# Kernel optimization log

Measured on AMD Instinct MI355X. Metric: run time of the kernel, lower is better.

## Reference

```python
import jax, jax.numpy as jnp
import numpy as np

B, L, IN, HID, D3 = 32, 8192, 512, 512, 128

def setup_inputs() -> dict:
    key = jax.random.key(0)
    ks = jax.random.split(key, 7)
    s_in = 1.0 / np.sqrt(IN)
    s_h = 1.0 / np.sqrt(HID)
    return {
        'inputs': jax.random.normal(ks[0], (B, IN), jnp.float32),
        'context': jax.random.normal(ks[1], (B, L, HID), jnp.float32),
        'Wi': jax.random.uniform(ks[2], (D3, IN), jnp.float32, -s_in, s_in),
        'bi': jax.random.uniform(ks[3], (D3,), jnp.float32, -s_in, s_in),
        'Wh': jax.random.uniform(ks[4], (D3, HID), jnp.float32, -s_h, s_h),
        'bh': jax.random.uniform(ks[5], (D3,), jnp.float32, -s_h, s_h),
        'V': jax.random.uniform(ks[6], (D3,), jnp.float32, -1.0, 1.0),
    }

def reference(inputs, context, Wi, bi, Wh, bh, V):
    # inputs: (B, IN) -> (B, 1, D3); context: (B, L, HID) -> (B, L, D3)
    q = (inputs @ Wi.T + bi)[:, None, :]
    k = jnp.einsum('blh,dh->bld', context, Wh) + bh
    a = jnp.tanh(q + k)                              # (B, L, D3)
    att_row = jnp.einsum('bld,d->bl', a, V)[:, None, :]  # (B, 1, L)
    # NOTE: original applies softmax over dim=1 (the singleton dim) -> all ones.
    att = jax.nn.softmax(att_row, axis=1).squeeze(1)     # (B, L), faithful quirk
    return (att_row, att)
```

## Files before the change

### kernel.cpp

```cpp
#include <hip/hip_runtime.h>

typedef __attribute__((ext_vector_type(8))) short short8;
typedef __attribute__((ext_vector_type(8))) unsigned short ushort8;
typedef __attribute__((ext_vector_type(4))) float f32x4;

#define B_   32
#define L_   8192
#define IN_  512
#define HID_ 512
#define D3_  128

static __device__ __forceinline__ short f2bf(float f) {
    return __builtin_bit_cast(short, (__bf16)f);
}
static __device__ __forceinline__ unsigned short f2bfu(float f) {
    return __builtin_bit_cast(unsigned short, (__bf16)f);
}

static __device__ __forceinline__ void gload_lds16(const void* g, void* l) {
    __builtin_amdgcn_global_load_lds(
        (const __attribute__((address_space(1))) unsigned int*)g,
        (__attribute__((address_space(3))) unsigned int*)l, 16, 0, 0);
}

__global__ void prep_whb2(const float* __restrict__ wh, unsigned short* __restrict__ whb2) {
    int u = blockIdx.x * 256 + threadIdx.x;
    int lane = u & 63;
    int nt   = (u >> 6) & 7;
    int ks   = u >> 9;
    int col  = nt * 16 + (lane & 15);
    int k0   = ks * 32 + (lane >> 4) * 8;
    const float* src = wh + col * HID_ + k0;
    float4 a = *(const float4*)(src);
    float4 b = *(const float4*)(src + 4);
    unsigned short* d = whb2 + (size_t)u * 8;
    d[0] = f2bfu(a.x); d[1] = f2bfu(a.y); d[2] = f2bfu(a.z); d[3] = f2bfu(a.w);
    d[4] = f2bfu(b.x); d[5] = f2bfu(b.y); d[6] = f2bfu(b.z); d[7] = f2bfu(b.w);
}

__global__ void prep_qpb(const float* __restrict__ inputs, const float* __restrict__ Wi,
                         const float* __restrict__ bi, const float* __restrict__ bh,
                         float* __restrict__ qpb) {
    int b = blockIdx.x;
    int d = threadIdx.x;
    float acc = bi[d] + bh[d];
    const float* xr = inputs + b * IN_;
    const float* wr = Wi + d * IN_;
    #pragma unroll 4
    for (int i = 0; i < IN_; i += 4) {
        float4 x = *(const float4*)(xr + i);
        float4 w = *(const float4*)(wr + i);
        acc += x.x * w.x + x.y * w.y + x.z * w.z + x.w * w.w;
    }
    qpb[b * D3_ + d] = acc;
}

__global__ __launch_bounds__(512) void attn_main(
    const float* __restrict__ ctx, const unsigned short* __restrict__ whb2,
    const float* __restrict__ qpb, const float* __restrict__ V,
    float* __restrict__ out)
{
    __shared__ unsigned short whs[D3_ * HID_];
    __shared__ float cbuf[2][4096];

    const int tid = threadIdx.x;

    #pragma unroll
    for (int p = 0; p < 16; ++p) {
        int m = p * 512 + tid;
        *(ushort8*)((char*)whs + (size_t)m * 16) = *(const ushort8*)(whb2 + (size_t)m * 8);
    }
    __syncthreads();

    const int lane = tid & 63;
    const int w    = tid >> 6;
    const int cb   = lane & 15;
    const int g    = lane >> 4;

    const char* bptr = (const char*)whs + lane * 16;

    const int srow = lane >> 3;
    const int spce = (lane & 7) ^ srow;
    const float* gsrcA = ctx
        + ((size_t)blockIdx.x * 1024 + w * 16 + srow) * (size_t)HID_ + spce * 4;
    const float* gsrcB = gsrcA + 8 * HID_;
    char* ldst = (char*)cbuf + w * 2048 + lane * 16;

    const char* abase = (const char*)cbuf + w * 2048 + (cb >> 3) * 1024 + (cb & 7) * 128;
    const int aoff0 = (((2 * g)     ^ (cb & 7)) << 4);
    const int aoff1 = (((2 * g + 1) ^ (cb & 7)) << 4);

    const int b = blockIdx.x >> 3;

    float vv[8], qv[8];
    #pragma unroll
    for (int nt = 0; nt < 8; ++nt) {
        vv[nt] = V[nt * 16 + cb];
        qv[nt] = qpb[b * D3_ + nt * 16 + cb];
    }

#define STAGE(CC) { \
    const size_t go_ = (size_t)((CC) >> 4) * (128 * HID_) + ((CC) & 15) * 32; \
    char* l0_ = ldst + (((CC) & 1) ? 16384 : 0); \
    gload_lds16(gsrcA + go_, l0_); \
    gload_lds16(gsrcB + go_, l0_ + 1024); }

    STAGE(0)
    STAGE(1)

    #pragma unroll 1
    for (int t = 0; t < 8; ++t) {
        f32x4 acc[8];
        #pragma unroll
        for (int nt = 0; nt < 8; ++nt) acc[nt] = (f32x4){0.f, 0.f, 0.f, 0.f};

        #pragma unroll
        for (int kk = 0; kk < 16; ++kk) {
            const int c = t * 16 + kk;
            if (c < 127) asm volatile("s_waitcnt vmcnt(2)" ::: "memory");
            else         asm volatile("s_waitcnt vmcnt(0)" ::: "memory");

            const char* ap = abase + ((c & 1) ? 16384 : 0);
            const f32x4 a0 = *(const f32x4*)(ap + aoff0);
            const f32x4 a1 = *(const f32x4*)(ap + aoff1);
            asm volatile("s_waitcnt lgkmcnt(0)" ::: "memory");
            __builtin_amdgcn_sched_barrier(0);
            if (c + 2 < 128) STAGE(c + 2)
            __builtin_amdgcn_sched_barrier(0);

            short8 aA;
            aA[0] = f2bf(a0[0]); aA[1] = f2bf(a0[1]); aA[2] = f2bf(a0[2]); aA[3] = f2bf(a0[3]);
            aA[4] = f2bf(a1[0]); aA[5] = f2bf(a1[1]); aA[6] = f2bf(a1[2]); aA[7] = f2bf(a1[3]);

            const char* bp = bptr + kk * 8192;
            #pragma unroll
            for (int nt = 0; nt < 8; ++nt) {
                const short8 bb = *(const short8*)(bp + nt * 1024);
                acc[nt] = __builtin_amdgcn_mfma_f32_16x16x32_bf16(aA, bb, acc[nt], 0, 0, 0);
            }

            if (kk == 15) {
                float s0 = 0.f, s1 = 0.f, s2 = 0.f, s3 = 0.f;
                #pragma unroll
                for (int nt = 0; nt < 8; ++nt) {
                    const float q = qv[nt], vn = vv[nt];
                    s0 += (1.f - 2.f / (__expf(2.f * (acc[nt][0] + q)) + 1.f)) * vn;
                    s1 += (1.f - 2.f / (__expf(2.f * (acc[nt][1] + q)) + 1.f)) * vn;
                    s2 += (1.f - 2.f / (__expf(2.f * (acc[nt][2] + q)) + 1.f)) * vn;
                    s3 += (1.f - 2.f / (__expf(2.f * (acc[nt][3] + q)) + 1.f)) * vn;
                }
                #pragma unroll
                for (int m = 1; m < 16; m <<= 1) {
                    s0 += __shfl_xor(s0, m, 64);
                    s1 += __shfl_xor(s1, m, 64);
                    s2 += __shfl_xor(s2, m, 64);
                    s3 += __shfl_xor(s3, m, 64);
                }
                if (cb == 0) {
                    const size_t row0 = (size_t)blockIdx.x * 1024 + (size_t)t * 128 + w * 16;
                    const size_t off_ = row0 + (size_t)g * 4;
                    *(float4*)(out + off_) = make_float4(s0, s1, s2, s3);
                    *(float4*)(out + (size_t)B_ * L_ + off_) = make_float4(1.f, 1.f, 1.f, 1.f);
                }
            }
        }
    }
#undef STAGE
}

extern "C" void kernel_launch(void* const* d_in, const int* in_sizes, int n_in,
                              void* d_out, int out_size, void* d_ws, size_t ws_size,
                              hipStream_t stream) {
    const float* inputs  = (const float*)d_in[0];
    const float* context = (const float*)d_in[1];
    const float* Wi      = (const float*)d_in[2];
    const float* bi      = (const float*)d_in[3];
    const float* Wh      = (const float*)d_in[4];
    const float* bh      = (const float*)d_in[5];
    const float* V       = (const float*)d_in[6];
    float* out = (float*)d_out;

    unsigned short* whb2 = (unsigned short*)d_ws;
    float* qpb = (float*)((char*)d_ws + (size_t)D3_ * HID_ * 2);

    prep_whb2<<<32, 256, 0, stream>>>(Wh, whb2);
    prep_qpb<<<B_, D3_, 0, stream>>>(inputs, Wi, bi, bh, qpb);
    attn_main<<<256, 512, 0, stream>>>(context, whb2, qpb, V, out);
}
```

Before: 124.6 us.

## Stream Wh weight windows through double-buffered LDS instead of preloading whole matrix

```diff
diff --git a/kernel.cpp b/kernel.cpp
--- a/kernel.cpp
+++ b/kernel.cpp
@@ -60,35 +60,29 @@
     const float* __restrict__ qpb, const float* __restrict__ V,
     float* __restrict__ out)
 {
-    __shared__ unsigned short whs[D3_ * HID_];
-    __shared__ float cbuf[2][4096];
-
-    const int tid = threadIdx.x;
-
-    #pragma unroll
-    for (int p = 0; p < 16; ++p) {
-        int m = p * 512 + tid;
-        *(ushort8*)((char*)whs + (size_t)m * 16) = *(const ushort8*)(whb2 + (size_t)m * 8);
-    }
-    __syncthreads();
-
+    __shared__ unsigned short bwin[2][16384];
+    __shared__ float cbuf[16384];
+
+    const int tid  = threadIdx.x;
     const int lane = tid & 63;
     const int w    = tid >> 6;
     const int cb   = lane & 15;
     const int g    = lane >> 4;
-
-    const char* bptr = (const char*)whs + lane * 16;
 
     const int srow = lane >> 3;
     const int spce = (lane & 7) ^ srow;
     const float* gsrcA = ctx
         + ((size_t)blockIdx.x * 1024 + w * 16 + srow) * (size_t)HID_ + spce * 4;
     const float* gsrcB = gsrcA + 8 * HID_;
-    char* ldst = (char*)cbuf + w * 2048 + lane * 16;
-
-    const char* abase = (const char*)cbuf + w * 2048 + (cb >> 3) * 1024 + (cb & 7) * 128;
+    char* ldstA = (char*)cbuf + w * 8192 + lane * 16;
+
+    const char* abase = (const char*)cbuf + w * 8192 + (cb >> 3) * 1024 + (cb & 7) * 128;
     const int aoff0 = (((2 * g)     ^ (cb & 7)) << 4);
     const int aoff1 = (((2 * g + 1) ^ (cb & 7)) << 4);
+
+    const char* bssrc = (const char*)whb2 + w * 1024 + lane * 16;
+    char* bsdst = (char*)bwin + w * 1024 + lane * 16;
+    const char* bread = (const char*)bwin + lane * 16;
 
     const int b = blockIdx.x >> 3;
 
@@ -99,73 +93,97 @@
         qv[nt] = qpb[b * D3_ + nt * 16 + cb];
     }
 
-#define STAGE(CC) { \
-    const size_t go_ = (size_t)((CC) >> 4) * (128 * HID_) + ((CC) & 15) * 32; \
-    char* l0_ = ldst + (((CC) & 1) ? 16384 : 0); \
+#define STAGE_A(CC) { \
+    const int cc_ = (CC) & 127; \
+    const size_t go_ = (size_t)(cc_ >> 4) * (128 * HID_) + (cc_ & 15) * 32; \
+    char* l0_ = ldstA + ((CC) & 3) * 2048; \
     gload_lds16(gsrcA + go_, l0_); \
     gload_lds16(gsrcB + go_, l0_ + 1024); }
 
-    STAGE(0)
-    STAGE(1)
+#define STAGE_B(WN) { \
+    const int kw_ = ((WN) & 3) * 4; \
+    char* d_ = bsdst + ((WN) & 1) * 32768; \
+    gload_lds16(bssrc + (size_t)(kw_ + 0) * 8192, d_); \
+    gload_lds16(bssrc + (size_t)(kw_ + 1) * 8192, d_ + 8192); \
+    gload_lds16(bssrc + (size_t)(kw_ + 2) * 8192, d_ + 16384); \
+    gload_lds16(bssrc + (size_t)(kw_ + 3) * 8192, d_ + 24576); }
+
+    STAGE_A(0) STAGE_A(1) STAGE_A(2) STAGE_A(3)
+    STAGE_B(0)
+    asm volatile("s_waitcnt vmcnt(8)" ::: "memory");
+    __builtin_amdgcn_s_barrier();
+
+    f32x4 acc[8];
 
     #pragma unroll 1
-    for (int t = 0; t < 8; ++t) {
-        f32x4 acc[8];
+    for (int W = 0; W < 32; ++W) {
+        if ((W & 3) == 0) {
+            #pragma unroll
+            for (int nt = 0; nt < 8; ++nt) acc[nt] = (f32x4){0.f, 0.f, 0.f, 0.f};
+        }
+
+        __builtin_amdgcn_sched_barrier(0);
+        STAGE_B(W + 1)
+        __builtin_amdgcn_sched_barrier(0);
+
+        const char* bwp = bread + (W & 1) * 32768;
         #pragma unroll
-        for (int nt = 0; nt < 8; ++nt) acc[nt] = (f32x4){0.f, 0.f, 0.f, 0.f};
-
-        #pragma unroll
-        for (int kk = 0; kk < 16; ++kk) {
-            const int c = t * 16 + kk;
-            if (c < 127) asm volatile("s_waitcnt vmcnt(2)" ::: "memory");
-            else         asm volatile("s_waitcnt vmcnt(0)" ::: "memory");
-
-            const char* ap = abase + ((c & 1) ? 16384 : 0);
+        for (int j = 0; j < 4; ++j) {
+            asm volatile("s_waitcnt vmcnt(10)" ::: "memory");
+            __builtin_amdgcn_sched_barrier(0);
+
+            const char* ap = abase + j * 2048;
             const f32x4 a0 = *(const f32x4*)(ap + aoff0);
             const f32x4 a1 = *(const f32x4*)(ap + aoff1);
             asm volatile("s_waitcnt lgkmcnt(0)" ::: "memory");
             __builtin_amdgcn_sched_barrier(0);
-            if (c + 2 < 128) STAGE(c + 2)
+            STAGE_A(4 * W + j + 4)
             __builtin_amdgcn_sched_barrier(0);
 
             short8 aA;
             aA[0] = f2bf(a0[0]); aA[1] = f2bf(a0[1]); aA[2] = f2bf(a0[2]); aA[3] = f2bf(a0[3]);
             aA[4] = f2bf(a1[0]); aA[5] = f2bf(a1[1]); aA[6] = f2bf(a1[2]); aA[7] = f2bf(a1[3]);
 
-            const char* bp = bptr + kk * 8192;
+            const char* bp = bwp + j * 8192;
             #pragma unroll
             for (int nt = 0; nt < 8; ++nt) {
                 const short8 bb = *(const short8*)(bp + nt * 1024);
                 acc[nt] = __builtin_amdgcn_mfma_f32_16x16x32_bf16(aA, bb, acc[nt], 0, 0, 0);
             }
-
-            if (kk == 15) {
-                float s0 = 0.f, s1 = 0.f, s2 = 0.f, s3 = 0.f;
-                #pragma unroll
-                for (int nt = 0; nt < 8; ++nt) {
-                    const float q = qv[nt], vn = vv[nt];
-                    s0 += (1.f - 2.f / (__expf(2.f * (acc[nt][0] + q)) + 1.f)) * vn;
-                    s1 += (1.f - 2.f / (__expf(2.f * (acc[nt][1] + q)) + 1.f)) * vn;
-                    s2 += (1.f - 2.f / (__expf(2.f * (acc[nt][2] + q)) + 1.f)) * vn;
-                    s3 += (1.f - 2.f / (__expf(2.f * (acc[nt][3] + q)) + 1.f)) * vn;
-                }
-                #pragma unroll
-                for (int m = 1; m < 16; m <<= 1) {
-                    s0 += __shfl_xor(s0, m, 64);
-                    s1 += __shfl_xor(s1, m, 64);
-                    s2 += __shfl_xor(s2, m, 64);
-                    s3 += __shfl_xor(s3, m, 64);
-                }
-                if (cb == 0) {
-                    const size_t row0 = (size_t)blockIdx.x * 1024 + (size_t)t * 128 + w * 16;
-                    const size_t off_ = row0 + (size_t)g * 4;
-                    *(float4*)(out + off_) = make_float4(s0, s1, s2, s3);
-                    *(float4*)(out + (size_t)B_ * L_ + off_) = make_float4(1.f, 1.f, 1.f, 1.f);
-                }
-            }
         }
+
+        if ((W & 3) == 3) {
+            float s0 = 0.f, s1 = 0.f, s2 = 0.f, s3 = 0.f;
+            #pragma unroll
+            for (int nt = 0; nt < 8; ++nt) {
+                const float q = qv[nt], vn = vv[nt];
+                s0 += (1.f - 2.f / (__expf(2.f * (acc[nt][0] + q)) + 1.f)) * vn;
+                s1 += (1.f - 2.f / (__expf(2.f * (acc[nt][1] + q)) + 1.f)) * vn;
+                s2 += (1.f - 2.f / (__expf(2.f * (acc[nt][2] + q)) + 1.f)) * vn;
+                s3 += (1.f - 2.f / (__expf(2.f * (acc[nt][3] + q)) + 1.f)) * vn;
+            }
+            #pragma unroll
+            for (int m = 1; m < 16; m <<= 1) {
+                s0 += __shfl_xor(s0, m, 64);
+                s1 += __shfl_xor(s1, m, 64);
+                s2 += __shfl_xor(s2, m, 64);
+                s3 += __shfl_xor(s3, m, 64);
+            }
+            if (cb == 0) {
+                const size_t row0 = (size_t)blockIdx.x * 1024 + (size_t)(W >> 2) * 128 + w * 16;
+                const size_t off_ = row0 + (size_t)g * 4;
+                *(float4*)(out + off_) = make_float4(s0, s1, s2, s3);
+                *(float4*)(out + (size_t)B_ * L_ + off_) = make_float4(1.f, 1.f, 1.f, 1.f);
+            }
+        }
+
+        asm volatile("s_waitcnt vmcnt(8)" ::: "memory");
+        asm volatile("s_waitcnt lgkmcnt(0)" ::: "memory");
+        __builtin_amdgcn_sched_barrier(0);
+        __builtin_amdgcn_s_barrier();
     }
-#undef STAGE
+#undef STAGE_A
+#undef STAGE_B
 }
 
 extern "C" void kernel_launch(void* const* d_in, const int* in_sizes, int n_in,
```

New measurement: 145.4 us. 16.7% more time.
